# Optimization experiments

Hardware: AMD Instinct MI355X
Metric: run time of the kernel (lower is better)

Reference implementation:

```python
import jax, jax.numpy as jnp
import numpy as np

N, T, E, B = 50000, 16, 800000, 2000
EMB, ENC, DEC, OUT_LEN = 32, 64, 128, 25
NEG_SLOPE = 0.1
BN_EPS = 1e-5


def lrelu(x):
    return jnp.where(x >= 0, x, NEG_SLOPE * x)


def gru_encode(xs, Wih, Whh, bih, bhh):
    # xs: [T, N, in] -> final hidden [N, H]   (torch GRU gate order: r, z, n)
    H = Whh.shape[1]

    def step(h, x_t):
        gi = x_t @ Wih.T + bih
        gh = h @ Whh.T + bhh
        i_r, i_z, i_n = jnp.split(gi, 3, axis=-1)
        h_r, h_z, h_n = jnp.split(gh, 3, axis=-1)
        r = jax.nn.sigmoid(i_r + h_r)
        z = jax.nn.sigmoid(i_z + h_z)
        n = jnp.tanh(i_n + r * h_n)
        return (1.0 - z) * n + z * h, None

    h0 = jnp.zeros((xs.shape[1], H), xs.dtype)
    hT, _ = jax.lax.scan(step, h0, xs)
    return hT


def lstm_layer(xs, Wih, Whh, bih, bhh):
    # xs: [T, B, in] -> outputs [T, B, H]   (torch LSTM gate order: i, f, g, o)
    H = Whh.shape[1]

    def step(carry, x_t):
        h, c = carry
        g = x_t @ Wih.T + bih + h @ Whh.T + bhh
        i, f, gg, o = jnp.split(g, 4, axis=-1)
        c = jax.nn.sigmoid(f) * c + jax.nn.sigmoid(i) * jnp.tanh(gg)
        h = jax.nn.sigmoid(o) * jnp.tanh(c)
        return (h, c), h

    z0 = jnp.zeros((xs.shape[1], H), xs.dtype)
    _, hs = jax.lax.scan(step, (z0, z0), xs)
    return hs


def cgconv(x, src, dst, edge_attr, Wf, bf, Ws, bs, gamma, beta, mean, var):
    # PyG CGConv: z = [x_i, x_j, e]; msg = sigmoid(lin_f(z)) * softplus(lin_s(z));
    # out = x + BN(scatter_add(msg, i))
    z = jnp.concatenate([x[dst], x[src], edge_attr], axis=-1)  # [E, 2*ENC+2]
    msg = jax.nn.sigmoid(z @ Wf.T + bf) * jax.nn.softplus(z @ Ws.T + bs)
    agg = jax.ops.segment_sum(msg, dst, num_segments=N)  # [N, ENC]
    agg = (agg - mean) * jax.lax.rsqrt(var + BN_EPS) * gamma + beta
    return x + agg


def setup_inputs() -> dict:
    key = jax.random.key(0)
    ks = jax.random.split(key, 32)

    def rn(k, shape, scale=0.1):
        return jax.random.normal(k, shape, jnp.float32) * scale

    inp = {}
    inp["x"] = jax.random.normal(ks[0], (N, T, 2), jnp.float32)
    inp["edge_index"] = jax.random.randint(ks[1], (2, E), 0, N)
    inp["edge_attr"] = jax.random.normal(ks[2], (E, 2), jnp.float32)
    inp["target_index"] = jnp.sort(jax.random.randint(ks[3], (B,), 0, N))
    inp["W_ip"] = rn(ks[4], (EMB, 2)); inp["b_ip"] = jnp.zeros((EMB,), jnp.float32)
    inp["gru_Wih"] = rn(ks[5], (3 * ENC, EMB)); inp["gru_Whh"] = rn(ks[6], (3 * ENC, ENC))
    inp["gru_bih"] = jnp.zeros((3 * ENC,), jnp.float32); inp["gru_bhh"] = jnp.zeros((3 * ENC,), jnp.float32)
    inp["W_dyn"] = rn(ks[7], (ENC, ENC)); inp["b_dyn"] = jnp.zeros((ENC,), jnp.float32)
    Z = 2 * ENC + 2
    for i, base in ((1, 8), (2, 14)):
        inp[f"cg{i}_Wf"] = rn(ks[base], (ENC, Z)); inp[f"cg{i}_bf"] = jnp.zeros((ENC,), jnp.float32)
        inp[f"cg{i}_Ws"] = rn(ks[base + 1], (ENC, Z)); inp[f"cg{i}_bs"] = jnp.zeros((ENC,), jnp.float32)
        inp[f"cg{i}_gamma"] = jnp.ones((ENC,), jnp.float32); inp[f"cg{i}_beta"] = jnp.zeros((ENC,), jnp.float32)
        inp[f"cg{i}_mean"] = jnp.zeros((ENC,), jnp.float32); inp[f"cg{i}_var"] = jnp.ones((ENC,), jnp.float32)
    inp["W_nbrs"] = rn(ks[20], (ENC, ENC)); inp["b_nbrs"] = jnp.zeros((ENC,), jnp.float32)
    inp["lstm0_Wih"] = rn(ks[21], (4 * DEC, 2 * ENC)); inp["lstm0_Whh"] = rn(ks[22], (4 * DEC, DEC))
    inp["lstm0_bih"] = jnp.zeros((4 * DEC,), jnp.float32); inp["lstm0_bhh"] = jnp.zeros((4 * DEC,), jnp.float32)
    inp["lstm1_Wih"] = rn(ks[23], (4 * DEC, DEC)); inp["lstm1_Whh"] = rn(ks[24], (4 * DEC, DEC))
    inp["lstm1_bih"] = jnp.zeros((4 * DEC,), jnp.float32); inp["lstm1_bhh"] = jnp.zeros((4 * DEC,), jnp.float32)
    inp["W_op"] = rn(ks[25], (2, DEC)); inp["b_op"] = jnp.zeros((2,), jnp.float32)
    return inp


def reference(x, edge_index, edge_attr, target_index, W_ip, b_ip,
              gru_Wih, gru_Whh, gru_bih, gru_bhh, W_dyn, b_dyn,
              cg1_Wf, cg1_bf, cg1_Ws, cg1_bs, cg1_gamma, cg1_beta, cg1_mean, cg1_var,
              cg2_Wf, cg2_bf, cg2_Ws, cg2_bs, cg2_gamma, cg2_beta, cg2_mean, cg2_var,
              W_nbrs, b_nbrs,
              lstm0_Wih, lstm0_Whh, lstm0_bih, lstm0_bhh,
              lstm1_Wih, lstm1_Whh, lstm1_bih, lstm1_bhh, W_op, b_op):
    src, dst = edge_index[0], edge_index[1]
    # --- history encoder (GRU) ---
    h = lrelu(x @ W_ip.T + b_ip)                                  # [N, T, EMB]
    hT = gru_encode(h.transpose(1, 0, 2), gru_Wih, gru_Whh, gru_bih, gru_bhh)  # [N, ENC]
    hist = lrelu(lrelu(hT) @ W_dyn.T + b_dyn)                     # [N, ENC]
    # --- CGConv interaction x2 ---
    f = cgconv(hist, src, dst, edge_attr, cg1_Wf, cg1_bf, cg1_Ws, cg1_bs,
               cg1_gamma, cg1_beta, cg1_mean, cg1_var)
    f = cgconv(f, src, dst, edge_attr, cg2_Wf, cg2_bf, cg2_Ws, cg2_bs,
               cg2_gamma, cg2_beta, cg2_mean, cg2_var)
    tar = lrelu(f[target_index] @ W_nbrs.T + b_nbrs)              # [B, ENC]
    enc = jnp.concatenate([hist[target_index], tar], axis=-1)     # [B, 2*ENC]
    # --- LSTM decoder over repeated encoding ---
    xs = jnp.broadcast_to(enc, (OUT_LEN,) + enc.shape)            # [OUT_LEN, B, 2*ENC]
    hs = lstm_layer(xs, lstm0_Wih, lstm0_Whh, lstm0_bih, lstm0_bhh)
    hs = lstm_layer(hs, lstm1_Wih, lstm1_Whh, lstm1_bih, lstm1_bhh)
    fut = hs.transpose(1, 0, 2) @ W_op.T + b_op                   # [B, OUT_LEN, 2]
    return fut
```

## Files before the change

kernel.cpp:

```cpp
#include <hip/hip_runtime.h>
#include <math.h>

#define NN   50000
#define TT   16
#define EE   800000
#define BB   2000
#define EMBD 32
#define ENC  64
#define DEC  128
#define OUTL 25
#define BN_EPS 1e-5f

typedef short v8s __attribute__((ext_vector_type(8)));
typedef float v4f __attribute__((ext_vector_type(4)));
#define MFMA16(a,b,c) __builtin_amdgcn_mfma_f32_16x16x32_bf16((a),(b),(c),0,0,0)

__device__ __forceinline__ float lrelu(float v){ return v >= 0.f ? v : 0.1f*v; }
__device__ __forceinline__ float fsig(float v){ return __builtin_amdgcn_rcpf(1.f + __expf(-v)); }
__device__ __forceinline__ float ftanh(float v){ return 2.f*__builtin_amdgcn_rcpf(1.f + __expf(-2.f*v)) - 1.f; }
__device__ __forceinline__ float fsoftplus(float v){
    return v > 15.f ? v : __logf(1.f + __expf(v));
}
__device__ __forceinline__ float hsum(float4 a){ return (a.x+a.y)+(a.z+a.w); }

__device__ __forceinline__ unsigned short f2bf(float f){
    unsigned u = __float_as_uint(f);
    u = u + 0x7FFFu + ((u>>16)&1u);
    return (unsigned short)(u>>16);
}
__device__ __forceinline__ float bf2f(unsigned short s){ return __uint_as_float(((unsigned)s)<<16); }

__device__ __forceinline__ void tsplit(float v, unsigned short& hi, unsigned short& lo){
    unsigned u = __float_as_uint(v);
    hi = (unsigned short)(u >> 16);
    float r = v - __uint_as_float(u & 0xFFFF0000u);
    lo = (unsigned short)(__float_as_uint(r) >> 16);
}

__device__ __forceinline__ v8s as_v8s(int4 v){
    union { int4 i; v8s s; } u; u.i = v; return u.s;
}

__device__ __forceinline__ void cvt8(const float* p, v8s& hi, v8s& lo){
    float4 a0 = *(const float4*)p;
    float4 a1 = *(const float4*)(p+4);
    float av[8] = {a0.x,a0.y,a0.z,a0.w,a1.x,a1.y,a1.z,a1.w};
#pragma unroll
    for (int j=0;j<8;j++){
        unsigned short h = f2bf(av[j]);
        hi[j] = (short)h;
        lo[j] = (short)f2bf(av[j] - bf2f(h));
    }
}
__device__ __forceinline__ void lrelu_resplit(v8s hh, v8s hl, v8s& oh, v8s& ol){
#pragma unroll
    for (int j=0;j<8;j++){
        float v = bf2f((unsigned short)hh[j]) + bf2f((unsigned short)hl[j]);
        float a = lrelu(v);
        unsigned short h = f2bf(a);
        oh[j] = (short)h;
        ol[j] = (short)f2bf(a - bf2f(h));
    }
}

__device__ __forceinline__ void pf_item(const float* W, int K, int KB, int i,
                                        unsigned short* out){
    int l = i & 63, fb = i >> 6;
    int kb = fb % KB, nt = fb / KB;
    int n = nt*16 + (l&15);
    int k0 = kb*32 + ((l>>4)*8);
#pragma unroll
    for (int j=0;j<8;j++) out[i*8+j] = f2bf(W[(size_t)n*K + k0 + j]);
}
__device__ __forceinline__ void phl_item(const float* W, int K, int KB, int i,
                                         unsigned short* hi, unsigned short* lo){
    int l = i & 63, fb = i >> 6;
    int kb = fb % KB, nt = fb / KB;
    int n = nt*16 + (l&15);
    int k0 = kb*32 + ((l>>4)*8);
#pragma unroll
    for (int j=0;j<8;j++){
        float v = W[(size_t)n*K + k0 + j];
        unsigned short h = f2bf(v);
        hi[i*8+j] = h;
        lo[i*8+j] = f2bf(v - bf2f(h));
    }
}
__device__ __forceinline__ void pcat_item(const float* Wa, const float* Wb,
                                          int K1, int K, int KB, int i,
                                          unsigned short* out){
    int l = i & 63, fb = i >> 6;
    int kb = fb % KB, nt = fb / KB;
    int n = nt*16 + (l&15);
    int k0 = kb*32 + ((l>>4)*8);
#pragma unroll
    for (int j=0;j<8;j++){
        int k = k0 + j;
        float v = (k < K1) ? Wa[(size_t)n*K1 + k] : Wb[(size_t)n*(K-K1) + (k-K1)];
        out[i*8+j] = f2bf(v);
    }
}
__device__ __forceinline__ void pproj_item(const float* Wf, const float* Ws, int i,
                                           unsigned short* hi, unsigned short* lo){
    int l = i & 63, fb = i >> 6;
    int kb = fb & 1, nt = fb >> 1;
    int n = nt*16 + (l&15);
    int d = n >> 6, c = n & 63;
    const float* W = (d < 2) ? Wf : Ws;
    int k0 = (d&1)*64 + kb*32 + ((l>>4)*8);
#pragma unroll
    for (int j=0;j<8;j++){
        float v = W[c*130 + k0 + j];
        unsigned short h = f2bf(v);
        hi[i*8+j] = h;
        lo[i*8+j] = f2bf(v - bf2f(h));
    }
}

__global__ void pack_all(
    const float* __restrict__ gWih, const float* __restrict__ gWhh,
    const float* __restrict__ Wdyn,
    const float* __restrict__ l0Whh, const float* __restrict__ l1Wih,
    const float* __restrict__ l1Whh, const float* __restrict__ l0Wih,
    const float* __restrict__ c1Wf, const float* __restrict__ c1Ws,
    const float* __restrict__ c2Wf, const float* __restrict__ c2Ws,
    unsigned short* __restrict__ pWih, unsigned short* __restrict__ pWhh,
    unsigned short* __restrict__ pWdyn,
    unsigned short* __restrict__ B0h, unsigned short* __restrict__ B1h,
    unsigned short* __restrict__ P1h, unsigned short* __restrict__ P1l,
    unsigned short* __restrict__ P2h, unsigned short* __restrict__ P2l,
    unsigned short* __restrict__ GIh, unsigned short* __restrict__ GIl,
    int* __restrict__ cnt, int* __restrict__ gtot)
{
    int i = blockIdx.x*256 + threadIdx.x;
    if (i < 768){ pf_item(gWih, 32, 1, i, pWih); return; }   i -= 768;
    if (i < 1536){ pf_item(gWhh, 64, 2, i, pWhh); return; }  i -= 1536;
    if (i < 512){ pf_item(Wdyn, 64, 2, i, pWdyn); return; }  i -= 512;
    if (i < 8192){ pcat_item(l0Whh, l0Whh, 128, 128, 4, i, B0h); return; } i -= 8192;
    if (i < 16384){ pcat_item(l1Wih, l1Whh, 128, 256, 8, i, B1h); return; } i -= 16384;
    if (i < 2048){ pproj_item(c1Wf, c1Ws, i, P1h, P1l); return; } i -= 2048;
    if (i < 2048){ pproj_item(c2Wf, c2Ws, i, P2h, P2l); return; } i -= 2048;
    if (i < 8192){ phl_item(l0Wih, 128, 4, i, GIh, GIl); return; } i -= 8192;
    if (i < NN){ cnt[i] = 0; return; } i -= NN;
    if (i < 1){ gtot[0] = 0; return; }
}
#define PACK_TOTAL (768+1536+512+8192+16384+2048+2048+8192+NN+1)

__global__ __launch_bounds__(64) void encoder_mfma(
    const float* __restrict__ x,
    const float* __restrict__ Wip, const float* __restrict__ bip,
    const unsigned short* __restrict__ pWih,
    const unsigned short* __restrict__ pWhh,
    const float* __restrict__ bih, const float* __restrict__ bhh,
    const unsigned short* __restrict__ pWdyn,
    const float* __restrict__ bdyn,
    float* __restrict__ hist)
{
    __shared__ float sxt[512];
    __shared__ unsigned short hfh[1024], hfl[1024];
    const int tid = threadIdx.x;
    const int l   = tid;
    const int ln  = l & 15, q = l >> 4;
    const int blk = blockIdx.x;

    for (int idx = tid; idx < 512; idx += 64){
        int m = idx >> 5, r = idx & 31;
        sxt[(r>>1)*32 + m*2 + (r&1)] = x[(size_t)blk*512 + idx];
    }
    for (int i = tid; i < 1024; i += 64){ hfh[i] = 0; hfl[i] = 0; }

    float w0[8], w1[8], bk[8];
#pragma unroll
    for (int j = 0; j < 8; j++){
        int k = q*8 + j;
        w0[j] = Wip[2*k]; w1[j] = Wip[2*k+1]; bk[j] = bip[k];
    }

    float bR[4], bZ[4], bNI[4], bNH[4];
    float hprev[4][4];
#pragma unroll
    for (int g = 0; g < 4; g++){
        int c = g*16 + ln;
        bR[g]  = bih[c]       + bhh[c];
        bZ[g]  = bih[64 + c]  + bhh[64 + c];
        bNI[g] = bih[128 + c];
        bNH[g] = bhh[128 + c];
        hprev[g][0]=0.f; hprev[g][1]=0.f; hprev[g][2]=0.f; hprev[g][3]=0.f;
    }
    const v8s* FIH = (const v8s*)pWih;
    const v8s* FHH = (const v8s*)pWhh;
    const v8s* FDY = (const v8s*)pWdyn;
    __syncthreads();

#pragma unroll 1
    for (int t = 0; t < TT; t++){
        float2 xv = *(const float2*)&sxt[t*32 + ln*2];
        v8s eh, el;
#pragma unroll
        for (int j = 0; j < 8; j++){
            float e = lrelu(w0[j]*xv.x + w1[j]*xv.y + bk[j]);
            unsigned short h_, l_;
            tsplit(e, h_, l_);
            eh[j] = (short)h_; el[j] = (short)l_;
        }
        v8s h0h = *(const v8s*)&hfh[l*8];
        v8s h0l = *(const v8s*)&hfl[l*8];
        v8s h1h = *(const v8s*)&hfh[512 + l*8];
        v8s h1l = *(const v8s*)&hfl[512 + l*8];
#pragma unroll
        for (int g = 0; g < 4; g++){
            v4f aR = {bR[g],bR[g],bR[g],bR[g]};
            v4f aZ = {bZ[g],bZ[g],bZ[g],bZ[g]};
            v4f aNI= {bNI[g],bNI[g],bNI[g],bNI[g]};
            v4f aNH= {bNH[g],bNH[g],bNH[g],bNH[g]};
            v8s b;
            b = FIH[(g   )*64 + l];    aR = MFMA16(eh,b,aR);  aR = MFMA16(el,b,aR);
            b = FHH[(g*2+0)*64+l];     aR = MFMA16(h0h,b,aR); aR = MFMA16(h0l,b,aR);
            b = FHH[(g*2+1)*64+l];     aR = MFMA16(h1h,b,aR); aR = MFMA16(h1l,b,aR);
            b = FIH[(4+g )*64 + l];    aZ = MFMA16(eh,b,aZ);  aZ = MFMA16(el,b,aZ);
            b = FHH[((4+g)*2+0)*64+l]; aZ = MFMA16(h0h,b,aZ); aZ = MFMA16(h0l,b,aZ);
            b = FHH[((4+g)*2+1)*64+l]; aZ = MFMA16(h1h,b,aZ); aZ = MFMA16(h1l,b,aZ);
            b = FIH[(8+g )*64 + l];    aNI= MFMA16(eh,b,aNI); aNI= MFMA16(el,b,aNI);
            b = FHH[((8+g)*2+0)*64+l]; aNH= MFMA16(h0h,b,aNH);aNH= MFMA16(h0l,b,aNH);
            b = FHH[((8+g)*2+1)*64+l]; aNH= MFMA16(h1h,b,aNH);aNH= MFMA16(h1l,b,aNH);
#pragma unroll
            for (int i = 0; i < 4; i++){
                float r_ = fsig(aR[i]);
                float z_ = fsig(aZ[i]);
                float nn_ = ftanh(aNI[i] + r_*aNH[i]);
                float hn = (1.f - z_)*nn_ + z_*hprev[g][i];
                hprev[g][i] = hn;
                int row = q*4 + i, col = g*16 + ln;
                int off = (col>>5)*512 + (16*((col&31)>>3) + row)*8 + (col&7);
                unsigned short hh_, hl_;
                tsplit(hn, hh_, hl_);
                hfh[off] = hh_;
                hfl[off] = hl_;
            }
        }
        __syncthreads();
    }
    {
        v8s a0h,a0l,a1h,a1l;
        lrelu_resplit(*(const v8s*)&hfh[l*8],       *(const v8s*)&hfl[l*8],       a0h, a0l);
        lrelu_resplit(*(const v8s*)&hfh[512 + l*8], *(const v8s*)&hfl[512 + l*8], a1h, a1l);
#pragma unroll
        for (int nt = 0; nt < 4; nt++){
            float bb = bdyn[nt*16 + ln];
            v4f acc = {bb,bb,bb,bb};
            v8s b;
            b = FDY[(nt*2+0)*64 + l]; acc = MFMA16(a0h,b,acc); acc = MFMA16(a0l,b,acc);
            b = FDY[(nt*2+1)*64 + l]; acc = MFMA16(a1h,b,acc); acc = MFMA16(a1l,b,acc);
#pragma unroll
            for (int i = 0; i < 4; i++){
                hist[(size_t)(blk*16 + q*4 + i)*64 + nt*16 + ln] = lrelu(acc[i]);
            }
        }
    }
}

__global__ __launch_bounds__(256) void proj_mfma(
    const float* __restrict__ xin,
    const unsigned short* __restrict__ Bh, const unsigned short* __restrict__ Bl,
    float* __restrict__ Af, float* __restrict__ Bf,
    float* __restrict__ As, float* __restrict__ Bs)
{
    __shared__ float sx[64*68];
    const int tid = threadIdx.x;
    const int l = tid & 63;
    const int w = tid >> 6;
    const int ln = l & 15, q = l >> 4;
    const int n0 = blockIdx.x*64;

    for (int i=tid;i<64*16;i+=256){
        int nn = i>>4, f4 = i&15;
        float4 v = {0.f,0.f,0.f,0.f};
        if (n0+nn < NN) v = ((const float4*)(xin + (size_t)(n0+nn)*64))[f4];
        *(float4*)&sx[nn*68 + f4*4] = v;
    }
    __syncthreads();

    v8s ah0,al0,ah1,al1;
    cvt8(&sx[(w*16+ln)*68 +      q*8], ah0, al0);
    cvt8(&sx[(w*16+ln)*68 + 32 + q*8], ah1, al1);

    const v8s* FH = (const v8s*)Bh;
    const v8s* FL = (const v8s*)Bl;
#pragma unroll 1
    for (int nt=0; nt<16; nt++){
        v8s bh0 = FH[(nt*2+0)*64 + l], bl0 = FL[(nt*2+0)*64 + l];
        v8s bh1 = FH[(nt*2+1)*64 + l], bl1 = FL[(nt*2+1)*64 + l];
        v4f acc = {0.f,0.f,0.f,0.f};
        acc = MFMA16(ah0,bh0,acc); acc = MFMA16(al0,bh0,acc); acc = MFMA16(ah0,bl0,acc);
        acc = MFMA16(ah1,bh1,acc); acc = MFMA16(al1,bh1,acc); acc = MFMA16(ah1,bl1,acc);
        int d = nt >> 2, col = (nt&3)*16 + ln;
        float* op = (d==0) ? Af : (d==1) ? Bf : (d==2) ? As : Bs;
#pragma unroll
        for (int i=0;i<4;i++){
            int node = n0 + w*16 + q*4 + i;
            if (node < NN) op[(size_t)node*64 + col] = acc[i];
        }
    }
}

__global__ void count_kernel(const int* __restrict__ ei, int* __restrict__ cnt){
    int e = blockIdx.x*256 + threadIdx.x;
    if (e < EE) atomicAdd(&cnt[ei[EE+e]], 1);
}

__global__ void alloc_kernel(const int* __restrict__ cnt, int* __restrict__ gtot,
                             int* __restrict__ off, int* __restrict__ cur){
    int n = blockIdx.x*256 + threadIdx.x;
    if (n >= NN) return;
    int c = cnt[n];
    int s = atomicAdd(gtot, c);
    off[n] = s;
    cur[n] = s;
}

__global__ void scatter_kernel(const int* __restrict__ ei, const float* __restrict__ ea,
                               int* __restrict__ cur, int4* __restrict__ recS){
    int e = blockIdx.x*256 + threadIdx.x;
    if (e >= EE) return;
    int d = ei[EE+e];
    int p = atomicAdd(&cur[d], 1);
    int4 r;
    r.x = ei[e];
    r.y = __float_as_int(ea[2*(size_t)e]);
    r.z = __float_as_int(ea[2*(size_t)e+1]);
    r.w = 0;
    recS[p] = r;
}

__global__ __launch_bounds__(256) void cg_agg(
    const float* __restrict__ xin,
    const int4* __restrict__ recS,
    const int* __restrict__ off, const int* __restrict__ cnt,
    const float* __restrict__ Wf, const float* __restrict__ bf,
    const float* __restrict__ Ws, const float* __restrict__ bs,
    const float* __restrict__ Af, const float* __restrict__ Bf,
    const float* __restrict__ As, const float* __restrict__ Bs,
    const float* __restrict__ gamma, const float* __restrict__ beta,
    const float* __restrict__ mean, const float* __restrict__ var,
    float* __restrict__ outp)
{
    const int tid = threadIdx.x;
    const int c = tid & 63, wid = tid >> 6;
    const int n = blockIdx.x*4 + wid;
    if (n >= NN) return;

    const float wf0 = Wf[c*130+128], wf1 = Wf[c*130+129], bfc = bf[c];
    const float ws0 = Ws[c*130+128], ws1 = Ws[c*130+129], bsc = bs[c];
    const float afd = Af[(size_t)n*64+c] + bfc, asd = As[(size_t)n*64+c] + bsc;
    const float* Bfc = Bf + c;
    const float* Bsc = Bs + c;

    float acc = 0.f;
    int i = off[n];
    const int i1 = i + cnt[n];
#pragma unroll 1
    for (; i+1 < i1; i += 2){
        int4 r0 = recS[i], r1 = recS[i+1];
        float e00 = __int_as_float(r0.y), e01 = __int_as_float(r0.z);
        float e10 = __int_as_float(r1.y), e11 = __int_as_float(r1.z);
        float bf0v = Bfc[(size_t)r0.x*64], bs0v = Bsc[(size_t)r0.x*64];
        float bf1v = Bfc[(size_t)r1.x*64], bs1v = Bsc[(size_t)r1.x*64];
        float gf0 = afd + bf0v + wf0*e00 + wf1*e01;
        float gs0 = asd + bs0v + ws0*e00 + ws1*e01;
        float gf1 = afd + bf1v + wf0*e10 + wf1*e11;
        float gs1 = asd + bs1v + ws0*e10 + ws1*e11;
        acc += fsig(gf0)*fsoftplus(gs0);
        acc += fsig(gf1)*fsoftplus(gs1);
    }
    if (i < i1){
        int4 r0 = recS[i];
        float e00 = __int_as_float(r0.y), e01 = __int_as_float(r0.z);
        float gf = afd + Bfc[(size_t)r0.x*64] + wf0*e00 + wf1*e01;
        float gs = asd + Bsc[(size_t)r0.x*64] + ws0*e00 + ws1*e01;
        acc += fsig(gf)*fsoftplus(gs);
    }
    float bn = (acc - mean[c])*rsqrtf(var[c]+BN_EPS)*gamma[c] + beta[c];
    outp[(size_t)n*64+c] = xin[(size_t)n*64+c] + bn;
}

__global__ __launch_bounds__(256) void target_kernel(
    const float* __restrict__ hist, const float* __restrict__ f2,
    const int* __restrict__ tgt,
    const float* __restrict__ Wn, const float* __restrict__ bn_,
    float* __restrict__ enc)
{
    const int tid=threadIdx.x;
    const int c = tid&63, q = tid>>6;
    const int b = blockIdx.x*4 + q;
    if (b>=BB) return;
    const int n = tgt[b];
    float a = bn_[c];
#pragma unroll
    for (int k=0;k<ENC;k++) a += Wn[c*64+k]*f2[(size_t)n*64+k];
    enc[(size_t)b*128 + 64 + c] = lrelu(a);
    enc[(size_t)b*128 + c]      = hist[(size_t)n*64+c];
}

__global__ __launch_bounds__(512) void gi0_mfma(
    const float* __restrict__ enc,
    const unsigned short* __restrict__ GIh, const unsigned short* __restrict__ GIl,
    const float* __restrict__ bih0, const float* __restrict__ bhh0,
    float* __restrict__ gi0)
{
    __shared__ float senc[16*132];
    const int tid = threadIdx.x;
    const int l = tid & 63;
    const int w = tid >> 6;
    const int ln = l & 15, q = l >> 4;
    const int b0 = blockIdx.x*16;

    for (int i=tid;i<16*32;i+=512){
        int row = i>>5, f4 = i&31;
        *(float4*)&senc[row*132 + f4*4] = ((const float4*)(enc + (size_t)(b0+row)*128))[f4];
    }
    __syncthreads();

    v8s ah[4], al[4];
#pragma unroll
    for (int kb=0;kb<4;kb++) cvt8(&senc[ln*132 + kb*32 + q*8], ah[kb], al[kb]);

    const v8s* FH = (const v8s*)GIh;
    const v8s* FL = (const v8s*)GIl;
#pragma unroll
    for (int u=0;u<4;u++){
        int nt = w*4 + u;
        int col = nt*16 + ln;
        float bb = bih0[col] + bhh0[col];
        v4f acc = {bb,bb,bb,bb};
#pragma unroll
        for (int kb=0;kb<4;kb++){
            v8s bh = FH[(nt*4+kb)*64 + l];
            v8s bl = FL[(nt*4+kb)*64 + l];
            acc = MFMA16(ah[kb],bh,acc); acc = MFMA16(al[kb],bh,acc); acc = MFMA16(ah[kb],bl,acc);
        }
#pragma unroll
        for (int i=0;i<4;i++)
            gi0[(size_t)(b0 + q*4 + i)*512 + col] = acc[i];
    }
}

#define LMB 16
__global__ __launch_bounds__(512)
__attribute__((amdgpu_waves_per_eu(2,2)))
void lstm_mfma(
    const float* __restrict__ gi0,
    const unsigned short* __restrict__ B0h,
    const unsigned short* __restrict__ B1h,
    const float* __restrict__ bih1, const float* __restrict__ bhh1,
    const float* __restrict__ Wop, const float* __restrict__ bop,
    float* __restrict__ outp)
{
    __shared__ int4 sW0[32*4*64];
    __shared__ unsigned short h0hi[2][4*512], h0lo[2][4*512];
    __shared__ unsigned short h1hi[2][4*512], h1lo[2][4*512];
    const int tid = threadIdx.x;
    const int l = tid & 63;
    const int w = tid >> 6;
    const int c = l & 15;
    const int q = l >> 4;
    const int j = w*16 + c;
    const int b0 = blockIdx.x*LMB;

    {
        const int4* F0 = (const int4*)B0h;
        for (int i=tid;i<32*4*64;i+=512) sW0[i] = F0[i];
    }
    for (int i=tid;i<4*512;i+=512){
        h0hi[0][i]=0; h0lo[0][i]=0; h0hi[1][i]=0; h0lo[1][i]=0;
        h1hi[0][i]=0; h1lo[0][i]=0; h1hi[1][i]=0; h1lo[1][i]=0;
    }

    int4 W1r[32];
    {
        const int4* F1 = (const int4*)B1h;
#pragma unroll
        for (int g=0;g<4;g++)
#pragma unroll
            for (int kb=0;kb<8;kb++) W1r[g*8+kb] = F1[((g*8+w)*8 + kb)*64 + l];
#pragma unroll
        for (int i=0;i<32;i++)
            asm volatile("" : "+v"(W1r[i].x), "+v"(W1r[i].y), "+v"(W1r[i].z), "+v"(W1r[i].w));
    }

    float rgi[4][4];
#pragma unroll
    for (int g=0;g<4;g++)
#pragma unroll
        for (int i=0;i<4;i++)
            rgi[g][i] = gi0[(size_t)(b0 + q*4 + i)*512 + g*128 + j];

    float b1[4];
#pragma unroll
    for (int g=0;g<4;g++) b1[g] = bih1[g*128+j] + bhh1[g*128+j];
    float c0[4] = {0,0,0,0}, c1[4] = {0,0,0,0};
    const float wop0 = Wop[j], wop1 = Wop[128 + j];
    const float bo0 = bop[0], bo1 = bop[1];
    const int kbw = j>>5, qw = (j>>3)&3, jw = j&7;
    __syncthreads();

    int p = 0;
#pragma unroll 1
    for (int t=0;t<OUTL;t++){
        v4f aH[4], aL[4];
#pragma unroll
        for (int g=0;g<4;g++){
            v4f t4 = {rgi[g][0], rgi[g][1], rgi[g][2], rgi[g][3]};
            aH[g] = t4;
            v4f z = {0.f,0.f,0.f,0.f};
            aL[g] = z;
        }
#pragma unroll
        for (int kb=0;kb<4;kb++){
            v8s ah = *(const v8s*)&h0hi[p][kb*512 + l*8];
            v8s al = *(const v8s*)&h0lo[p][kb*512 + l*8];
#pragma unroll
            for (int g=0;g<4;g++){
                v8s bfr = as_v8s(sW0[((g*8+w)*4 + kb)*64 + l]);
                aH[g] = MFMA16(ah, bfr, aH[g]);
                aL[g] = MFMA16(al, bfr, aL[g]);
            }
        }
#pragma unroll
        for (int i=0;i<4;i++){
            float gi_ = aH[0][i]+aL[0][i], gf_ = aH[1][i]+aL[1][i];
            float gg_ = aH[2][i]+aL[2][i], go_ = aH[3][i]+aL[3][i];
            c0[i] = fsig(gf_)*c0[i] + fsig(gi_)*ftanh(gg_);
            float hn = fsig(go_)*ftanh(c0[i]);
            int off = kbw*512 + (qw*16 + q*4 + i)*8 + jw;
            unsigned short h = f2bf(hn);
            h0hi[1-p][off] = h;
            h0lo[1-p][off] = f2bf(hn - bf2f(h));
        }
        __syncthreads();

        v4f bH[4], bL[4];
#pragma unroll
        for (int g=0;g<4;g++){
            v4f t4={b1[g],b1[g],b1[g],b1[g]}; bH[g]=t4;
            v4f z={0.f,0.f,0.f,0.f}; bL[g]=z;
        }
#pragma unroll
        for (int kb=0;kb<8;kb++){
            const unsigned short* hb = (kb<4) ? h0hi[1-p] : h1hi[p];
            const unsigned short* lb = (kb<4) ? h0lo[1-p] : h1lo[p];
            int kk = kb & 3;
            v8s ah = *(const v8s*)&hb[kk*512 + l*8];
            v8s al = *(const v8s*)&lb[kk*512 + l*8];
#pragma unroll
            for (int g=0;g<4;g++){
                bH[g] = MFMA16(ah, as_v8s(W1r[g*8+kb]), bH[g]);
                bL[g] = MFMA16(al, as_v8s(W1r[g*8+kb]), bL[g]);
            }
        }
        float h1new[4];
#pragma unroll
        for (int i=0;i<4;i++){
            float gi_ = bH[0][i]+bL[0][i], gf_ = bH[1][i]+bL[1][i];
            float gg_ = bH[2][i]+bL[2][i], go_ = bH[3][i]+bL[3][i];
            c1[i] = fsig(gf_)*c1[i] + fsig(gi_)*ftanh(gg_);
            h1new[i] = fsig(go_)*ftanh(c1[i]);
            int off = kbw*512 + (qw*16 + q*4 + i)*8 + jw;
            unsigned short h = f2bf(h1new[i]);
            h1hi[1-p][off] = h;
            h1lo[1-p][off] = f2bf(h1new[i] - bf2f(h));
        }

        {
            float v0[4], v1[4];
#pragma unroll
            for (int i=0;i<4;i++){ v0[i] = h1new[i]*wop0; v1[i] = h1new[i]*wop1; }
#pragma unroll
            for (int m=1;m<16;m<<=1){
#pragma unroll
                for (int i=0;i<4;i++){
                    v0[i] += __shfl_xor(v0[i], m);
                    v1[i] += __shfl_xor(v1[i], m);
                }
            }
            if (c == 0){
                if (w == 0){
#pragma unroll
                    for (int i=0;i<4;i++){ v0[i] += bo0; v1[i] += bo1; }
                }
#pragma unroll
                for (int i=0;i<4;i++){
                    size_t base = (size_t)(b0 + q*4 + i)*(OUTL*2) + t*2;
                    atomicAdd(&outp[base    ], v0[i]);
                    atomicAdd(&outp[base + 1], v1[i]);
                }
            }
        }
        p ^= 1;
    }
}

extern "C" void kernel_launch(void* const* d_in, const int* in_sizes, int n_in,
                              void* d_out, int out_size, void* d_ws, size_t ws_size,
                              hipStream_t stream)
{
    const float* x    = (const float*)d_in[0];
    const int*   ei   = (const int*)d_in[1];
    const float* ea   = (const float*)d_in[2];
    const int*   tgt  = (const int*)d_in[3];
    const float* Wip  = (const float*)d_in[4];
    const float* bip  = (const float*)d_in[5];
    const float* gWih = (const float*)d_in[6];
    const float* gWhh = (const float*)d_in[7];
    const float* gbih = (const float*)d_in[8];
    const float* gbhh = (const float*)d_in[9];
    const float* Wdyn = (const float*)d_in[10];
    const float* bdyn = (const float*)d_in[11];
    const float* c1Wf=(const float*)d_in[12]; const float* c1bf=(const float*)d_in[13];
    const float* c1Ws=(const float*)d_in[14]; const float* c1bs=(const float*)d_in[15];
    const float* c1g =(const float*)d_in[16]; const float* c1b =(const float*)d_in[17];
    const float* c1m =(const float*)d_in[18]; const float* c1v =(const float*)d_in[19];
    const float* c2Wf=(const float*)d_in[20]; const float* c2bf=(const float*)d_in[21];
    const float* c2Ws=(const float*)d_in[22]; const float* c2bs=(const float*)d_in[23];
    const float* c2g =(const float*)d_in[24]; const float* c2b =(const float*)d_in[25];
    const float* c2m =(const float*)d_in[26]; const float* c2v =(const float*)d_in[27];
    const float* Wn  =(const float*)d_in[28]; const float* bn_ =(const float*)d_in[29];
    const float* l0Wih=(const float*)d_in[30]; const float* l0Whh=(const float*)d_in[31];
    const float* l0bih=(const float*)d_in[32]; const float* l0bhh=(const float*)d_in[33];
    const float* l1Wih=(const float*)d_in[34]; const float* l1Whh=(const float*)d_in[35];
    const float* l1bih=(const float*)d_in[36]; const float* l1bhh=(const float*)d_in[37];
    const float* Wop =(const float*)d_in[38]; const float* bop=(const float*)d_in[39];

    float* ws = (float*)d_ws;
    size_t o = 0;
    float* hist = ws + o; o += (size_t)NN*ENC;
    float* f1   = ws + o; o += (size_t)NN*ENC;
    float* f2   = ws + o; o += (size_t)NN*ENC;
    float* Af   = ws + o; o += (size_t)NN*ENC;
    float* Bf   = ws + o; o += (size_t)NN*ENC;
    float* As   = ws + o; o += (size_t)NN*ENC;
    float* Bs   = ws + o; o += (size_t)NN*ENC;
    float* enc  = ws + o; o += (size_t)BB*2*ENC;
    float* gi0  = ws + o; o += (size_t)BB*4*DEC;
    unsigned short* pWih  = (unsigned short*)(ws + o); o += (size_t)12*64*8/2;
    unsigned short* pWhh  = (unsigned short*)(ws + o); o += (size_t)24*64*8/2;
    unsigned short* pWdyn = (unsigned short*)(ws + o); o += (size_t)8*64*8/2;
    unsigned short* B0h = (unsigned short*)(ws + o); o += (size_t)32*4*64*8/2;
    unsigned short* B1h = (unsigned short*)(ws + o); o += (size_t)32*8*64*8/2;
    unsigned short* P1h = (unsigned short*)(ws + o); o += (size_t)2048*8/2;
    unsigned short* P1l = (unsigned short*)(ws + o); o += (size_t)2048*8/2;
    unsigned short* P2h = (unsigned short*)(ws + o); o += (size_t)2048*8/2;
    unsigned short* P2l = (unsigned short*)(ws + o); o += (size_t)2048*8/2;
    unsigned short* GIh = (unsigned short*)(ws + o); o += (size_t)8192*8/2;
    unsigned short* GIl = (unsigned short*)(ws + o); o += (size_t)8192*8/2;
    int* cnt    = (int*)(ws + o); o += NN;
    int* offv   = (int*)(ws + o); o += NN+1;
    int* curv   = (int*)(ws + o); o += NN;
    int* gtot   = (int*)(ws + o); o += 1;
    o = (o + 3) & ~(size_t)3;
    int4* recS  = (int4*)(ws + o); o += (size_t)4*EE;

    pack_all<<<(PACK_TOTAL+255)/256, 256, 0, stream>>>(
        gWih, gWhh, Wdyn, l0Whh, l1Wih, l1Whh, l0Wih,
        c1Wf, c1Ws, c2Wf, c2Ws,
        pWih, pWhh, pWdyn, B0h, B1h, P1h, P1l, P2h, P2l, GIh, GIl, cnt, gtot);

    (void)hipMemsetAsync(d_out, 0, (size_t)out_size*sizeof(float), stream);

    count_kernel<<<(EE+255)/256, 256, 0, stream>>>(ei, cnt);
    alloc_kernel<<<(NN+255)/256, 256, 0, stream>>>(cnt, gtot, offv, curv);
    scatter_kernel<<<(EE+255)/256, 256, 0, stream>>>(ei, ea, curv, recS);

    encoder_mfma<<<NN/16, 64, 0, stream>>>(x, Wip, bip, pWih, pWhh, gbih, gbhh, pWdyn, bdyn, hist);

    proj_mfma<<<(NN+63)/64, 256, 0, stream>>>(hist, P1h, P1l, Af,Bf,As,Bs);
    cg_agg<<<(NN+3)/4, 256, 0, stream>>>(hist, recS, offv, cnt,
                                         c1Wf,c1bf,c1Ws,c1bs, Af,Bf,As,Bs,
                                         c1g,c1b,c1m,c1v, f1);

    proj_mfma<<<(NN+63)/64, 256, 0, stream>>>(f1, P2h, P2l, Af,Bf,As,Bs);
    cg_agg<<<(NN+3)/4, 256, 0, stream>>>(f1, recS, offv, cnt,
                                         c2Wf,c2bf,c2Ws,c2bs, Af,Bf,As,Bs,
                                         c2g,c2b,c2m,c2v, f2);

    target_kernel<<<(BB+3)/4, 256, 0, stream>>>(hist, f2, tgt, Wn, bn_, enc);

    gi0_mfma<<<BB/16, 512, 0, stream>>>(enc, GIh, GIl, l0bih, l0bhh, gi0);

    lstm_mfma<<<BB/LMB, 512, 0, stream>>>(gi0, B0h, B1h,
                                          l1bih, l1bhh, Wop, bop, (float*)d_out);
}
```

Before: 640.4 us.

## Split GRU encoder gate groups across two waves with double-buffered hidden state

The GRU encoder block grows from one wavefront to two. Each wave computes half of the 16-column gate groups, which halves the serial MFMA chain per timestep. The hidden-state LDS buffer is double-buffered so that one barrier per step is enough even though waves now write state other waves read. The cost is more threads and LDS per block and more barrier synchronization between the two waves, while the input embedding is computed redundantly in both waves.

```diff
diff --git a/kernel.cpp b/kernel.cpp
--- a/kernel.cpp
+++ b/kernel.cpp
@@ -146,7 +146,7 @@
 }
 #define PACK_TOTAL (768+1536+512+8192+16384+2048+2048+8192+NN+1)
 
-__global__ __launch_bounds__(64) void encoder_mfma(
+__global__ __launch_bounds__(128) void encoder_mfma(
     const float* __restrict__ x,
     const float* __restrict__ Wip, const float* __restrict__ bip,
     const unsigned short* __restrict__ pWih,
@@ -157,17 +157,20 @@
     float* __restrict__ hist)
 {
     __shared__ float sxt[512];
-    __shared__ unsigned short hfh[1024], hfl[1024];
+    __shared__ unsigned short hfh[2][1024], hfl[2][1024];
     const int tid = threadIdx.x;
-    const int l   = tid;
+    const int l   = tid & 63;
+    const int w   = tid >> 6;
     const int ln  = l & 15, q = l >> 4;
     const int blk = blockIdx.x;
 
-    for (int idx = tid; idx < 512; idx += 64){
+    for (int idx = tid; idx < 512; idx += 128){
         int m = idx >> 5, r = idx & 31;
         sxt[(r>>1)*32 + m*2 + (r&1)] = x[(size_t)blk*512 + idx];
     }
-    for (int i = tid; i < 1024; i += 64){ hfh[i] = 0; hfl[i] = 0; }
+    for (int i = tid; i < 1024; i += 128){
+        hfh[0][i]=0; hfl[0][i]=0; hfh[1][i]=0; hfl[1][i]=0;
+    }
 
     float w0[8], w1[8], bk[8];
 #pragma unroll
@@ -176,22 +179,24 @@
         w0[j] = Wip[2*k]; w1[j] = Wip[2*k+1]; bk[j] = bip[k];
     }
 
-    float bR[4], bZ[4], bNI[4], bNH[4];
-    float hprev[4][4];
-#pragma unroll
-    for (int g = 0; g < 4; g++){
+    float bR[2], bZ[2], bNI[2], bNH[2];
+    float hprev[2][4];
+#pragma unroll
+    for (int u = 0; u < 2; u++){
+        int g = 2*w + u;
         int c = g*16 + ln;
-        bR[g]  = bih[c]       + bhh[c];
-        bZ[g]  = bih[64 + c]  + bhh[64 + c];
-        bNI[g] = bih[128 + c];
-        bNH[g] = bhh[128 + c];
-        hprev[g][0]=0.f; hprev[g][1]=0.f; hprev[g][2]=0.f; hprev[g][3]=0.f;
+        bR[u]  = bih[c]       + bhh[c];
+        bZ[u]  = bih[64 + c]  + bhh[64 + c];
+        bNI[u] = bih[128 + c];
+        bNH[u] = bhh[128 + c];
+        hprev[u][0]=0.f; hprev[u][1]=0.f; hprev[u][2]=0.f; hprev[u][3]=0.f;
     }
     const v8s* FIH = (const v8s*)pWih;
     const v8s* FHH = (const v8s*)pWhh;
     const v8s* FDY = (const v8s*)pWdyn;
     __syncthreads();
 
+    int p = 0;
 #pragma unroll 1
     for (int t = 0; t < TT; t++){
         float2 xv = *(const float2*)&sxt[t*32 + ln*2];
@@ -203,16 +208,17 @@
             tsplit(e, h_, l_);
             eh[j] = (short)h_; el[j] = (short)l_;
         }
-        v8s h0h = *(const v8s*)&hfh[l*8];
-        v8s h0l = *(const v8s*)&hfl[l*8];
-        v8s h1h = *(const v8s*)&hfh[512 + l*8];
-        v8s h1l = *(const v8s*)&hfl[512 + l*8];
-#pragma unroll
-        for (int g = 0; g < 4; g++){
-            v4f aR = {bR[g],bR[g],bR[g],bR[g]};
-            v4f aZ = {bZ[g],bZ[g],bZ[g],bZ[g]};
-            v4f aNI= {bNI[g],bNI[g],bNI[g],bNI[g]};
-            v4f aNH= {bNH[g],bNH[g],bNH[g],bNH[g]};
+        v8s h0h = *(const v8s*)&hfh[p][l*8];
+        v8s h0l = *(const v8s*)&hfl[p][l*8];
+        v8s h1h = *(const v8s*)&hfh[p][512 + l*8];
+        v8s h1l = *(const v8s*)&hfl[p][512 + l*8];
+#pragma unroll
+        for (int u = 0; u < 2; u++){
+            int g = 2*w + u;
+            v4f aR = {bR[u],bR[u],bR[u],bR[u]};
+            v4f aZ = {bZ[u],bZ[u],bZ[u],bZ[u]};
+            v4f aNI= {bNI[u],bNI[u],bNI[u],bNI[u]};
+            v4f aNH= {bNH[u],bNH[u],bNH[u],bNH[u]};
             v8s b;
             b = FIH[(g   )*64 + l];    aR = MFMA16(eh,b,aR);  aR = MFMA16(el,b,aR);
             b = FHH[(g*2+0)*64+l];     aR = MFMA16(h0h,b,aR); aR = MFMA16(h0l,b,aR);
@@ -228,24 +234,26 @@
                 float r_ = fsig(aR[i]);
                 float z_ = fsig(aZ[i]);
                 float nn_ = ftanh(aNI[i] + r_*aNH[i]);
-                float hn = (1.f - z_)*nn_ + z_*hprev[g][i];
-                hprev[g][i] = hn;
+                float hn = (1.f - z_)*nn_ + z_*hprev[u][i];
+                hprev[u][i] = hn;
                 int row = q*4 + i, col = g*16 + ln;
                 int off = (col>>5)*512 + (16*((col&31)>>3) + row)*8 + (col&7);
                 unsigned short hh_, hl_;
                 tsplit(hn, hh_, hl_);
-                hfh[off] = hh_;
-                hfl[off] = hl_;
+                hfh[1-p][off] = hh_;
+                hfl[1-p][off] = hl_;
             }
         }
         __syncthreads();
+        p ^= 1;
     }
     {
         v8s a0h,a0l,a1h,a1l;
-        lrelu_resplit(*(const v8s*)&hfh[l*8],       *(const v8s*)&hfl[l*8],       a0h, a0l);
-        lrelu_resplit(*(const v8s*)&hfh[512 + l*8], *(const v8s*)&hfl[512 + l*8], a1h, a1l);
-#pragma unroll
-        for (int nt = 0; nt < 4; nt++){
+        lrelu_resplit(*(const v8s*)&hfh[p][l*8],       *(const v8s*)&hfl[p][l*8],       a0h, a0l);
+        lrelu_resplit(*(const v8s*)&hfh[p][512 + l*8], *(const v8s*)&hfl[p][512 + l*8], a1h, a1l);
+#pragma unroll
+        for (int u = 0; u < 2; u++){
+            int nt = 2*w + u;
             float bb = bdyn[nt*16 + ln];
             v4f acc = {bb,bb,bb,bb};
             v8s b;
@@ -670,7 +678,7 @@
     alloc_kernel<<<(NN+255)/256, 256, 0, stream>>>(cnt, gtot, offv, curv);
     scatter_kernel<<<(EE+255)/256, 256, 0, stream>>>(ei, ea, curv, recS);
 
-    encoder_mfma<<<NN/16, 64, 0, stream>>>(x, Wip, bip, pWih, pWhh, gbih, gbhh, pWdyn, bdyn, hist);
+    encoder_mfma<<<NN/16, 128, 0, stream>>>(x, Wip, bip, pWih, pWhh, gbih, gbhh, pWdyn, bdyn, hist);
 
     proj_mfma<<<(NN+63)/64, 256, 0, stream>>>(hist, P1h, P1l, Af,Bf,As,Bs);
     cg_agg<<<(NN+3)/4, 256, 0, stream>>>(hist, recS, offv, cnt,
```

New measurement: 617.0 us. -3.7%, faster.
